# Optimization experiments

Measured on AMD Instinct MI355X. Metric: run time of the kernel, lower is better.

The kernel has to match this reference:

```python
import jax, jax.numpy as jnp
import numpy as np

E = 16        # n_routed_experts
TOP_K = 2
C = 768       # n_embd
I = 1536      # intermediate_size
B, T = 8, 2048


def setup_inputs() -> dict:
    key = jax.random.key(0)
    ks = jax.random.split(key, 9)
    s = 0.02  # init scale
    return {
        "x": jax.random.normal(ks[0], (B, T, C), jnp.float32),
        "w_gate": jax.random.normal(ks[1], (C, E), jnp.float32) * s,
        "expert_bias": jnp.zeros((E,), jnp.float32),
        "wg": jax.random.normal(ks[2], (E, C, I), jnp.float32) * s,
        "wu": jax.random.normal(ks[3], (E, C, I), jnp.float32) * s,
        "wd": jax.random.normal(ks[4], (E, I, C), jnp.float32) * s,
        "swg": jax.random.normal(ks[5], (C, I), jnp.float32) * s,
        "swu": jax.random.normal(ks[6], (C, I), jnp.float32) * s,
        "swd": jax.random.normal(ks[7], (I, C), jnp.float32) * s,
    }


def _expert(x, wg_e, wu_e, wd_e):
    # SwiGLU FFN: down(silu(gate(x)) * up(x))
    return (jax.nn.silu(x @ wg_e) * (x @ wu_e)) @ wd_e


def reference(x, w_gate, expert_bias, wg, wu, wd, swg, swu, swd):
    Bq, Tq, Cq = x.shape
    xf = x.reshape(-1, Cq)  # (N, C)
    n_tok = xf.shape[0]

    # shared experts (1 expert, divided by count=1)
    shared = _expert(xf, swg, swu, swd)

    # router: softmax over (logits + bias), top-k, renormalize
    logits = xf @ w_gate + expert_bias  # (N, E)
    probs = jax.nn.softmax(logits, axis=-1)
    topk_p, topk_i = jax.lax.top_k(probs, TOP_K)
    topk_p = topk_p / jnp.sum(topk_p, axis=-1, keepdims=True)

    # combine weights per expert: zero where expert not selected
    comb = jnp.zeros((n_tok, E), xf.dtype).at[
        jnp.arange(n_tok)[:, None], topk_i
    ].add(topk_p)  # (N, E)

    routed = jnp.zeros_like(xf)
    for e in range(E):  # fixed small expert count
        routed = routed + comb[:, e:e + 1] * _expert(xf, wg[e], wu[e], wd[e])

    return (shared + routed).reshape(Bq, Tq, Cq)
```

## Files before the change

kernel.cpp:

```cpp
#include <hip/hip_runtime.h>

typedef unsigned short u16;
typedef unsigned int u32;
typedef __attribute__((ext_vector_type(4))) float f32x4;
typedef __attribute__((ext_vector_type(8))) short short8;
typedef __attribute__((ext_vector_type(4))) u16 u16x4;
typedef __attribute__((ext_vector_type(8))) u16 u16x8;

#define N_TOK 16384
#define C_DIM 768
#define I_DIM 1536
#define N_EXP 16
#define TM 128
#define BK 64
#define MAXT 400
#define PASS_T 200

#define CI_COUNTS 0
#define CI_STARTS 32
#define CI_NTILES 64
#define CI_TILE_E 128
#define CI_ESLOT 2048
#define CI_TOKW 36864
#define CI_PERM 102400
#define CI_RW 153600

#define XB_OFF  1048576u
#define WGU_OFF 26214400u
#define WDP_OFF 106430464u
#define ACT_OFF 146538496u

__device__ __forceinline__ u16 f2bf(float f) {
  u32 x = __float_as_uint(f);
  return (u16)((x + 0x7FFFu + ((x >> 16) & 1u)) >> 16);
}
__device__ __forceinline__ float bf2f(u16 h) {
  return __uint_as_float(((u32)h) << 16);
}
__device__ __forceinline__ void dma16(const void* g, void* l) {
  __builtin_amdgcn_global_load_lds(
      (const __attribute__((address_space(1))) unsigned int*)g,
      (__attribute__((address_space(3))) unsigned int*)l, 16, 0, 0);
}

__global__ void convert_kernel(const float* __restrict__ wg, const float* __restrict__ wu,
                               const float* __restrict__ wd, const float* __restrict__ swg,
                               const float* __restrict__ swu, const float* __restrict__ swd,
                               u16* __restrict__ wgu, u16* __restrict__ wdp) {
  int bid = blockIdx.x;
  const float* src; u16* dst; int K, N, base_n;
  if (bid < 34 * 48) {
    int m = bid / 48, nb = bid % 48;
    int e = m >> 1, gu = m & 1;
    src = (e < N_EXP) ? ((gu ? wu : wg) + (size_t)e * C_DIM * I_DIM) : (gu ? swu : swg);
    dst = wgu + (size_t)m * (C_DIM * I_DIM);
    K = C_DIM; N = I_DIM; base_n = nb * 32;
  } else {
    int b2 = bid - 34 * 48;
    int e = b2 / 24, nb = b2 % 24;
    src = (e < N_EXP) ? (wd + (size_t)e * I_DIM * C_DIM) : swd;
    dst = wdp + (size_t)e * (I_DIM * C_DIM);
    K = I_DIM; N = C_DIM; base_n = nb * 32;
  }
  int tid = threadIdx.x, lane = tid & 63, wv = tid >> 6;
  int lsub = lane >> 3, lchk = lane & 7;
  int ng = base_n + wv * 8 + lsub;
  int c = lchk ^ (ng & 7);
  const float* s0 = src + ng;
  u16* drow = dst + (size_t)ng * K;
  for (int k0 = 0; k0 < K; k0 += 64) {
    u16x8 o;
#pragma unroll
    for (int j = 0; j < 8; j++)
      o[j] = f2bf(s0[(size_t)(k0 + c * 8 + j) * N]);
    *(u16x8*)&drow[k0 + lchk * 8] = o;
  }
}

__global__ void router_kernel(const float* __restrict__ x, const float* __restrict__ wgate,
                              const float* __restrict__ ebias, int* __restrict__ ctrl,
                              u16* __restrict__ xb) {
  __shared__ float xs[16 * 772];
  __shared__ float wgsT[16 * 772];
  __shared__ float lg[16 * 16];
  int tid = threadIdx.x;
  int tok0 = blockIdx.x * 16;
  const float4* xsrc = (const float4*)(x + (size_t)tok0 * C_DIM);
  const float4* wsrc = (const float4*)wgate;
#pragma unroll
  for (int j = 0; j < 12; j++) {
    int q = tid + j * 256;
    float4 v = xsrc[q];
    int tk = q / 192;
    int c4 = q - tk * 192;
    *(float4*)&xs[tk * 772 + c4 * 4] = v;
    u16x4 o; o.x = f2bf(v.x); o.y = f2bf(v.y); o.z = f2bf(v.z); o.w = f2bf(v.w);
    *(u16x4*)(xb + (size_t)tok0 * C_DIM + (size_t)q * 4) = o;
    float4 w = wsrc[q];
    int c = q >> 2, e0 = (q & 3) * 4;
    wgsT[(e0 + 0) * 772 + c] = w.x;
    wgsT[(e0 + 1) * 772 + c] = w.y;
    wgsT[(e0 + 2) * 772 + c] = w.z;
    wgsT[(e0 + 3) * 772 + c] = w.w;
  }
  __syncthreads();
  int tk = tid >> 4, e = tid & 15;
  float acc = ebias[e];
  const float4* xr = (const float4*)&xs[tk * 772];
  const float4* wr = (const float4*)&wgsT[e * 772];
#pragma unroll 4
  for (int c4 = 0; c4 < 192; c4++) {
    float4 xv = xr[c4], wv = wr[c4];
    acc = fmaf(xv.x, wv.x, fmaf(xv.y, wv.y, fmaf(xv.z, wv.z, fmaf(xv.w, wv.w, acc))));
  }
  lg[tk * 16 + e] = acc;
  __syncthreads();
  if (tid < 16) {
    int n = tok0 + tid;
    float l0 = -1e30f, l1 = -1e30f; int i0 = 0, i1 = 0;
#pragma unroll
    for (int j = 0; j < 16; j++) {
      float l = lg[tid * 16 + j];
      if (l > l0) { l1 = l0; i1 = i0; l0 = l; i0 = j; }
      else if (l > l1) { l1 = l; i1 = j; }
    }
    float e1 = __expf(l1 - l0);
    float inv = 1.f / (1.f + e1);
    int s0 = atomicAdd(&ctrl[CI_COUNTS + i0], 1);
    int s1 = atomicAdd(&ctrl[CI_COUNTS + i1], 1);
    ctrl[CI_ESLOT + 2 * n]     = (i0 << 24) | s0;
    ctrl[CI_ESLOT + 2 * n + 1] = (i1 << 24) | s1;
    float* tw = (float*)(ctrl + CI_TOKW);
    tw[2 * n] = inv; tw[2 * n + 1] = e1 * inv;
  }
}

__global__ void tiles_kernel(int* __restrict__ ctrl) {
  if (threadIdx.x != 0) return;
  int cnt[17];
#pragma unroll
  for (int e = 0; e < 16; e++) cnt[e] = ctrl[CI_COUNTS + e];
  cnt[16] = N_TOK;
  ctrl[CI_COUNTS + 16] = N_TOK;
  int cur = 0, T = 0;
  for (int e = 0; e <= 16; e++) {
    ctrl[CI_STARTS + e] = cur;
    int nt = (cnt[e] + TM - 1) >> 7;
    for (int i = 0; i < nt; i++) ctrl[CI_TILE_E + T++] = e;
    cur += nt << 7;
  }
  ctrl[CI_NTILES] = T;
}

__global__ void scatter_kernel(int* __restrict__ ctrl) {
  int n = blockIdx.x * 256 + threadIdx.x;
  const float* tw = (const float*)(ctrl + CI_TOKW);
  float* rw = (float*)(ctrl + CI_RW);
#pragma unroll
  for (int k = 0; k < 2; k++) {
    int es = ctrl[CI_ESLOT + 2 * n + k];
    int e = es >> 24;
    int slot = es & 0xFFFFFF;
    int row = ctrl[CI_STARTS + e] + slot;
    ctrl[CI_PERM + row] = n;
    rw[row] = tw[2 * n + k];
  }
  int srow = ctrl[CI_STARTS + 16] + n;
  ctrl[CI_PERM + srow] = n;
  rw[srow] = 1.0f;
}

__global__ __launch_bounds__(256, 2)
void gemm1_kernel(const u16* __restrict__ xb, const u16* __restrict__ wgu,
                  u16* __restrict__ act, const int* __restrict__ ctrl, int tile0) {
  __shared__ u16 Al[TM * BK];
  __shared__ u16 Bg[TM * BK];
  __shared__ u16 Bu[TM * BK];
  int t = tile0 + blockIdx.x;
  if (t >= ctrl[CI_NTILES]) return;
  int e = ctrl[CI_TILE_E + t];
  int row0 = t << 7;
  int row0l = blockIdx.x << 7;
  int col0 = blockIdx.y * TM;
  int seg_start = ctrl[CI_STARTS + e];
  bool sh = (e == N_EXP);
  const u16* G = wgu + (size_t)(2 * e) * (C_DIM * I_DIM);
  const u16* U = G + C_DIM * I_DIM;
  int row_lim = sh ? 0x7fffffff : (seg_start + ctrl[CI_COUNTS + e]);
  const int* perm = ctrl + CI_PERM;
  int tid = threadIdx.x;
  int lane = tid & 63, wv = tid >> 6;
  int lsub = lane >> 3;
  int lchk = lane & 7;
  int co = (lchk ^ lsub) * 8;
  const u16* aptr[4];
#pragma unroll
  for (int j = 0; j < 4; j++) {
    int r = row0 + wv * 32 + j * 8 + lsub;
    int tok = sh ? (r - seg_start) : ((r < row_lim) ? perm[r] : 0);
    aptr[j] = xb + (size_t)tok * C_DIM + co;
  }
  size_t boff = (size_t)(col0 + wv * 32 + lsub) * C_DIM + lchk * 8;
  int ldst = wv * 2048;

  f32x4 accg[4][4], accu[4][4];
#pragma unroll
  for (int m = 0; m < 4; m++)
#pragma unroll
    for (int n = 0; n < 4; n++) {
      f32x4 z = {0.f, 0.f, 0.f, 0.f};
      accg[m][n] = z; accu[m][n] = z;
    }
  int lr = lane & 15, lq = lane >> 4;
  int rh = (wv & 1) * 64, chh = (wv >> 1) * 64;

  for (int kk = 0; kk < C_DIM; kk += BK) {
#pragma unroll
    for (int j = 0; j < 4; j++) {
      dma16(aptr[j] + kk,                    Al + ldst + j * 512);
      dma16(G + boff + j * (8 * C_DIM) + kk, Bg + ldst + j * 512);
      dma16(U + boff + j * (8 * C_DIM) + kk, Bu + ldst + j * 512);
    }
    __syncthreads();
#pragma unroll
    for (int s = 0; s < 2; s++) {
      int cidx = s * 4 + lq;
      short8 af[4], bg_[4], bu_[4];
#pragma unroll
      for (int m = 0; m < 4; m++) {
        int r = rh + m * 16 + lr;
        af[m] = *(const short8*)&Al[r * 64 + ((cidx ^ (r & 7)) * 8)];
      }
#pragma unroll
      for (int n = 0; n < 4; n++) {
        int i = chh + n * 16 + lr;
        int off = i * 64 + ((cidx ^ (i & 7)) * 8);
        bg_[n] = *(const short8*)&Bg[off];
        bu_[n] = *(const short8*)&Bu[off];
      }
#pragma unroll
      for (int m = 0; m < 4; m++)
#pragma unroll
        for (int n = 0; n < 4; n++) {
          accg[m][n] = __builtin_amdgcn_mfma_f32_16x16x32_bf16(af[m], bg_[n], accg[m][n], 0, 0, 0);
          accu[m][n] = __builtin_amdgcn_mfma_f32_16x16x32_bf16(af[m], bu_[n], accu[m][n], 0, 0, 0);
        }
    }
    __syncthreads();
  }
#pragma unroll
  for (int m = 0; m < 4; m++)
#pragma unroll
    for (int n = 0; n < 4; n++)
#pragma unroll
      for (int rg = 0; rg < 4; rg++) {
        float g = accg[m][n][rg];
        float h = accu[m][n][rg];
        float a = g * (1.f / (1.f + __expf(-g))) * h;
        int r_loc = rh + m * 16 + lq * 4 + rg;
        int cl = col0 + chh + n * 16 + lr;
        act[(size_t)(row0l + r_loc) * I_DIM + cl] = f2bf(a);
      }
}

__global__ __launch_bounds__(256, 3)
void gemm2_kernel(const u16* __restrict__ act, const u16* __restrict__ wdp,
                  float* __restrict__ out, const int* __restrict__ ctrl, int tile0) {
  __shared__ u16 Al[TM * BK];
  __shared__ u16 Bl[TM * BK];
  int t = tile0 + blockIdx.x;
  if (t >= ctrl[CI_NTILES]) return;
  int e = ctrl[CI_TILE_E + t];
  int row0 = t << 7;
  int row0l = blockIdx.x << 7;
  int col0 = blockIdx.y * TM;
  const u16* D = wdp + (size_t)e * (I_DIM * C_DIM);
  int tid = threadIdx.x;
  int lane = tid & 63, wv = tid >> 6;
  int lsub = lane >> 3, lchk = lane & 7;
  int co = (lchk ^ lsub) * 8;
  const u16* abase = act + (size_t)(row0l + wv * 32 + lsub) * I_DIM + co;
  size_t boff = (size_t)(col0 + wv * 32 + lsub) * I_DIM + lchk * 8;
  int ldst = wv * 2048;

  f32x4 acc[4][4];
#pragma unroll
  for (int m = 0; m < 4; m++)
#pragma unroll
    for (int n = 0; n < 4; n++) {
      f32x4 z = {0.f, 0.f, 0.f, 0.f};
      acc[m][n] = z;
    }
  int lr = lane & 15, lq = lane >> 4;
  int rh = (wv & 1) * 64, chh = (wv >> 1) * 64;

  for (int kk = 0; kk < I_DIM; kk += BK) {
#pragma unroll
    for (int j = 0; j < 4; j++) {
      dma16(abase + (size_t)j * 8 * I_DIM + kk, Al + ldst + j * 512);
      dma16(D + boff + j * (8 * I_DIM) + kk,    Bl + ldst + j * 512);
    }
    __syncthreads();
#pragma unroll
    for (int s = 0; s < 2; s++) {
      int cidx = s * 4 + lq;
      short8 af[4], bf_[4];
#pragma unroll
      for (int m = 0; m < 4; m++) {
        int r = rh + m * 16 + lr;
        af[m] = *(const short8*)&Al[r * 64 + ((cidx ^ (r & 7)) * 8)];
      }
#pragma unroll
      for (int n = 0; n < 4; n++) {
        int i = chh + n * 16 + lr;
        bf_[n] = *(const short8*)&Bl[i * 64 + ((cidx ^ (i & 7)) * 8)];
      }
#pragma unroll
      for (int m = 0; m < 4; m++)
#pragma unroll
        for (int n = 0; n < 4; n++)
          acc[m][n] = __builtin_amdgcn_mfma_f32_16x16x32_bf16(af[m], bf_[n], acc[m][n], 0, 0, 0);
    }
    __syncthreads();
  }
  const int* perm = ctrl + CI_PERM;
  const float* rw = (const float*)(ctrl + CI_RW);
#pragma unroll
  for (int m = 0; m < 4; m++)
#pragma unroll
    for (int rg = 0; rg < 4; rg++) {
      int rgrow = row0 + rh + m * 16 + lq * 4 + rg;
      int tokn = perm[rgrow];
      if (tokn < 0) continue;
      float w = rw[rgrow];
      float* obase = out + (size_t)tokn * C_DIM + col0 + chh + lr;
#pragma unroll
      for (int n = 0; n < 4; n++)
        atomicAdd(obase + n * 16, acc[m][n][rg] * w);
    }
}

extern "C" void kernel_launch(void* const* d_in, const int* in_sizes, int n_in,
                              void* d_out, int out_size, void* d_ws, size_t ws_size,
                              hipStream_t stream) {
  (void)in_sizes; (void)n_in; (void)out_size; (void)ws_size;
  const float* x     = (const float*)d_in[0];
  const float* wgate = (const float*)d_in[1];
  const float* ebias = (const float*)d_in[2];
  const float* wg    = (const float*)d_in[3];
  const float* wu    = (const float*)d_in[4];
  const float* wd    = (const float*)d_in[5];
  const float* swg   = (const float*)d_in[6];
  const float* swu   = (const float*)d_in[7];
  const float* swd   = (const float*)d_in[8];
  float* out = (float*)d_out;
  char* ws = (char*)d_ws;
  int* ctrl = (int*)ws;
  u16* xb  = (u16*)(ws + XB_OFF);
  u16* wgu = (u16*)(ws + WGU_OFF);
  u16* wdp = (u16*)(ws + WDP_OFF);
  u16* act = (u16*)(ws + ACT_OFF);

  hipMemsetAsync(ws, 0, 256, stream);
  hipMemsetAsync(ws + (size_t)CI_PERM * 4, 0xFF, 51200 * 4, stream);
  hipMemsetAsync(d_out, 0, (size_t)N_TOK * C_DIM * 4, stream);
  router_kernel<<<N_TOK / 16, 256, 0, stream>>>(x, wgate, ebias, ctrl, xb);
  tiles_kernel<<<1, 64, 0, stream>>>(ctrl);
  scatter_kernel<<<N_TOK / 256, 256, 0, stream>>>(ctrl);
  convert_kernel<<<34 * 48 + 17 * 24, 256, 0, stream>>>(wg, wu, wd, swg, swu, swd, wgu, wdp);
  for (int p = 0; p < 2; p++) {
    gemm1_kernel<<<dim3(PASS_T, I_DIM / TM), 256, 0, stream>>>(xb, wgu, act, ctrl, p * PASS_T);
    gemm2_kernel<<<dim3(PASS_T, C_DIM / TM), 256, 0, stream>>>(act, wdp, out, ctrl, p * PASS_T);
  }
}
```

Baseline: 1.001 ms.

## Enlarge GEMM tiles to 256 rows, interleave gate/up weights, double-buffer LDS

```diff
diff --git a/kernel.cpp b/kernel.cpp
--- a/kernel.cpp
+++ b/kernel.cpp
@@ -11,10 +11,10 @@
 #define C_DIM 768
 #define I_DIM 1536
 #define N_EXP 16
-#define TM 128
+#define TM 256
 #define BK 64
-#define MAXT 400
-#define PASS_T 200
+#define MAXT 208
+#define PASS_T 104
 
 #define CI_COUNTS 0
 #define CI_STARTS 32
@@ -23,12 +23,15 @@
 #define CI_ESLOT 2048
 #define CI_TOKW 36864
 #define CI_PERM 102400
-#define CI_RW 153600
+#define CI_RW 155648
 
 #define XB_OFF  1048576u
 #define WGU_OFF 26214400u
 #define WDP_OFF 106430464u
 #define ACT_OFF 146538496u
+
+#define BAR() asm volatile("s_barrier" ::: "memory")
+#define WAITVM(N) asm volatile("s_waitcnt vmcnt(" #N ")" ::: "memory")
 
 __device__ __forceinline__ u16 f2bf(float f) {
   u32 x = __float_as_uint(f);
@@ -48,32 +51,39 @@
                                const float* __restrict__ swu, const float* __restrict__ swd,
                                u16* __restrict__ wgu, u16* __restrict__ wdp) {
   int bid = blockIdx.x;
-  const float* src; u16* dst; int K, N, base_n;
-  if (bid < 34 * 48) {
-    int m = bid / 48, nb = bid % 48;
-    int e = m >> 1, gu = m & 1;
-    src = (e < N_EXP) ? ((gu ? wu : wg) + (size_t)e * C_DIM * I_DIM) : (gu ? swu : swg);
-    dst = wgu + (size_t)m * (C_DIM * I_DIM);
-    K = C_DIM; N = I_DIM; base_n = nb * 32;
-  } else {
-    int b2 = bid - 34 * 48;
-    int e = b2 / 24, nb = b2 % 24;
-    src = (e < N_EXP) ? (wd + (size_t)e * I_DIM * C_DIM) : swd;
-    dst = wdp + (size_t)e * (I_DIM * C_DIM);
-    K = I_DIM; N = C_DIM; base_n = nb * 32;
-  }
   int tid = threadIdx.x, lane = tid & 63, wv = tid >> 6;
   int lsub = lane >> 3, lchk = lane & 7;
-  int ng = base_n + wv * 8 + lsub;
-  int c = lchk ^ (ng & 7);
-  const float* s0 = src + ng;
-  u16* drow = dst + (size_t)ng * K;
-  for (int k0 = 0; k0 < K; k0 += 64) {
-    u16x8 o;
-#pragma unroll
-    for (int j = 0; j < 8; j++)
-      o[j] = f2bf(s0[(size_t)(k0 + c * 8 + j) * N]);
-    *(u16x8*)&drow[k0 + lchk * 8] = o;
+  if (bid < 17 * 96) {
+    int e = bid / 96, nb = bid % 96;
+    int ng = nb * 32 + wv * 8 + lsub;
+    int gu = (ng >> 4) & 1;
+    int scol = ((ng >> 5) << 4) | (ng & 15);
+    const float* src = (e < N_EXP) ? ((gu ? wu : wg) + (size_t)e * C_DIM * I_DIM)
+                                   : (gu ? swu : swg);
+    u16* drow = wgu + ((size_t)e * (2 * I_DIM) + ng) * C_DIM;
+    int c = lchk ^ (ng & 7);
+    const float* s0 = src + scol;
+    for (int k0 = 0; k0 < C_DIM; k0 += 64) {
+      u16x8 o;
+#pragma unroll
+      for (int j = 0; j < 8; j++) o[j] = f2bf(s0[(size_t)(k0 + c * 8 + j) * I_DIM]);
+      *(u16x8*)&drow[k0 + lchk * 8] = o;
+    }
+  } else {
+    int b2 = bid - 17 * 96;
+    int e = b2 / 24, nb = b2 % 24;
+    const float* src = (e < N_EXP) ? (wd + (size_t)e * I_DIM * C_DIM) : swd;
+    u16* dst = wdp + (size_t)e * (I_DIM * C_DIM);
+    int ng = nb * 32 + wv * 8 + lsub;
+    int c = lchk ^ (ng & 7);
+    const float* s0 = src + ng;
+    u16* drow = dst + (size_t)ng * I_DIM;
+    for (int k0 = 0; k0 < I_DIM; k0 += 64) {
+      u16x8 o;
+#pragma unroll
+      for (int j = 0; j < 8; j++) o[j] = f2bf(s0[(size_t)(k0 + c * 8 + j) * C_DIM]);
+      *(u16x8*)&drow[k0 + lchk * 8] = o;
+    }
   }
 }
 
@@ -145,9 +155,9 @@
   int cur = 0, T = 0;
   for (int e = 0; e <= 16; e++) {
     ctrl[CI_STARTS + e] = cur;
-    int nt = (cnt[e] + TM - 1) >> 7;
+    int nt = (cnt[e] + TM - 1) >> 8;
     for (int i = 0; i < nt; i++) ctrl[CI_TILE_E + T++] = e;
-    cur += nt << 7;
+    cur += nt << 8;
   }
   ctrl[CI_NTILES] = T;
 }
@@ -170,118 +180,126 @@
   rw[srow] = 1.0f;
 }
 
-__global__ __launch_bounds__(256, 2)
+__global__ __launch_bounds__(512, 2)
 void gemm1_kernel(const u16* __restrict__ xb, const u16* __restrict__ wgu,
                   u16* __restrict__ act, const int* __restrict__ ctrl, int tile0) {
-  __shared__ u16 Al[TM * BK];
-  __shared__ u16 Bg[TM * BK];
-  __shared__ u16 Bu[TM * BK];
-  int t = tile0 + blockIdx.x;
-  if (t >= ctrl[CI_NTILES]) return;
-  int e = ctrl[CI_TILE_E + t];
-  int row0 = t << 7;
-  int row0l = blockIdx.x << 7;
-  int col0 = blockIdx.y * TM;
-  int seg_start = ctrl[CI_STARTS + e];
+  __shared__ u16 As[2][256 * 64];
+  __shared__ u16 Bs[2][256 * 64];
+  int tt = tile0 + blockIdx.x;
+  if (tt >= ctrl[CI_NTILES]) return;
+  int e = ctrl[CI_TILE_E + tt];
+  int row0 = tt << 8;
+  int row0l = blockIdx.x << 8;
+  int col0c = blockIdx.y << 8;
+  int seg = ctrl[CI_STARTS + e];
   bool sh = (e == N_EXP);
-  const u16* G = wgu + (size_t)(2 * e) * (C_DIM * I_DIM);
-  const u16* U = G + C_DIM * I_DIM;
-  int row_lim = sh ? 0x7fffffff : (seg_start + ctrl[CI_COUNTS + e]);
+  const u16* W = wgu + (size_t)e * (2 * I_DIM * C_DIM);
+  int rlim = sh ? 0x7fffffff : (seg + ctrl[CI_COUNTS + e]);
   const int* perm = ctrl + CI_PERM;
   int tid = threadIdx.x;
   int lane = tid & 63, wv = tid >> 6;
-  int lsub = lane >> 3;
-  int lchk = lane & 7;
+  int lsub = lane >> 3, lchk = lane & 7;
   int co = (lchk ^ lsub) * 8;
   const u16* aptr[4];
 #pragma unroll
   for (int j = 0; j < 4; j++) {
     int r = row0 + wv * 32 + j * 8 + lsub;
-    int tok = sh ? (r - seg_start) : ((r < row_lim) ? perm[r] : 0);
+    int tok = sh ? (r - seg) : ((r < rlim) ? perm[r] : 0);
     aptr[j] = xb + (size_t)tok * C_DIM + co;
   }
-  size_t boff = (size_t)(col0 + wv * 32 + lsub) * C_DIM + lchk * 8;
-  int ldst = wv * 2048;
-
-  f32x4 accg[4][4], accu[4][4];
-#pragma unroll
-  for (int m = 0; m < 4; m++)
+  const u16* bptr = W + (size_t)(col0c + wv * 32 + lsub) * C_DIM + lchk * 8;
+  int ldst = (wv * 32 + lsub) * 64 + lchk * 8;
+
+  f32x4 acc[8][4];
+#pragma unroll
+  for (int m = 0; m < 8; m++)
 #pragma unroll
     for (int n = 0; n < 4; n++) {
       f32x4 z = {0.f, 0.f, 0.f, 0.f};
-      accg[m][n] = z; accu[m][n] = z;
+      acc[m][n] = z;
     }
   int lr = lane & 15, lq = lane >> 4;
-  int rh = (wv & 1) * 64, chh = (wv >> 1) * 64;
-
-  for (int kk = 0; kk < C_DIM; kk += BK) {
-#pragma unroll
-    for (int j = 0; j < 4; j++) {
-      dma16(aptr[j] + kk,                    Al + ldst + j * 512);
-      dma16(G + boff + j * (8 * C_DIM) + kk, Bg + ldst + j * 512);
-      dma16(U + boff + j * (8 * C_DIM) + kk, Bu + ldst + j * 512);
-    }
-    __syncthreads();
-#pragma unroll
-    for (int s = 0; s < 2; s++) {
-      int cidx = s * 4 + lq;
-      short8 af[4], bg_[4], bu_[4];
-#pragma unroll
-      for (int m = 0; m < 4; m++) {
-        int r = rh + m * 16 + lr;
-        af[m] = *(const short8*)&Al[r * 64 + ((cidx ^ (r & 7)) * 8)];
+  int wr = wv >> 2, wc = wv & 3;
+
+  auto stage = [&](int kt, int slot) {
+    int kk = kt * BK;
+#pragma unroll
+    for (int j = 0; j < 4; j++) dma16(aptr[j] + kk, &As[slot][ldst + j * 512]);
+#pragma unroll
+    for (int j = 0; j < 4; j++)
+      dma16(bptr + (size_t)j * (8 * C_DIM) + kk, &Bs[slot][ldst + j * 512]);
+  };
+
+  stage(0, 0);
+  stage(1, 1);
+  WAITVM(8);
+  BAR();
+  for (int kt = 0; kt < C_DIM / BK; ++kt) {
+    const u16* Ab = As[kt & 1];
+    const u16* Bb = Bs[kt & 1];
+    __builtin_amdgcn_s_setprio(1);
+#pragma unroll
+    for (int s = 0; s < 2; ++s) {
+      int csh = ((s * 4 + lq) ^ (lr & 7)) * 8;
+      short8 bfr[4];
+#pragma unroll
+      for (int n = 0; n < 4; n++)
+        bfr[n] = *(const short8*)&Bb[(wc * 64 + n * 16 + lr) * 64 + csh];
+#pragma unroll
+      for (int mh = 0; mh < 2; ++mh) {
+        short8 afr[4];
+#pragma unroll
+        for (int mm = 0; mm < 4; mm++)
+          afr[mm] = *(const short8*)&Ab[(wr * 128 + mh * 64 + mm * 16 + lr) * 64 + csh];
+#pragma unroll
+        for (int mm = 0; mm < 4; mm++)
+#pragma unroll
+          for (int n = 0; n < 4; n++)
+            acc[mh * 4 + mm][n] = __builtin_amdgcn_mfma_f32_16x16x32_bf16(
+                afr[mm], bfr[n], acc[mh * 4 + mm][n], 0, 0, 0);
       }
-#pragma unroll
-      for (int n = 0; n < 4; n++) {
-        int i = chh + n * 16 + lr;
-        int off = i * 64 + ((cidx ^ (i & 7)) * 8);
-        bg_[n] = *(const short8*)&Bg[off];
-        bu_[n] = *(const short8*)&Bu[off];
+    }
+    __builtin_amdgcn_s_setprio(0);
+    BAR();
+    if (kt + 2 < C_DIM / BK) { stage(kt + 2, kt & 1); WAITVM(8); }
+    else { WAITVM(0); }
+    BAR();
+  }
+  int cb = (blockIdx.y << 7) + wc * 32;
+#pragma unroll
+  for (int m = 0; m < 8; m++)
+#pragma unroll
+    for (int np = 0; np < 2; np++)
+#pragma unroll
+      for (int rg = 0; rg < 4; rg++) {
+        float g = acc[m][2 * np][rg];
+        float h = acc[m][2 * np + 1][rg];
+        float a = g * (1.f / (1.f + __expf(-g))) * h;
+        int r_loc = wr * 128 + m * 16 + lq * 4 + rg;
+        act[(size_t)(row0l + r_loc) * I_DIM + cb + np * 16 + lr] = f2bf(a);
       }
-#pragma unroll
-      for (int m = 0; m < 4; m++)
-#pragma unroll
-        for (int n = 0; n < 4; n++) {
-          accg[m][n] = __builtin_amdgcn_mfma_f32_16x16x32_bf16(af[m], bg_[n], accg[m][n], 0, 0, 0);
-          accu[m][n] = __builtin_amdgcn_mfma_f32_16x16x32_bf16(af[m], bu_[n], accu[m][n], 0, 0, 0);
-        }
-    }
-    __syncthreads();
-  }
-#pragma unroll
-  for (int m = 0; m < 4; m++)
-#pragma unroll
-    for (int n = 0; n < 4; n++)
-#pragma unroll
-      for (int rg = 0; rg < 4; rg++) {
-        float g = accg[m][n][rg];
-        float h = accu[m][n][rg];
-        float a = g * (1.f / (1.f + __expf(-g))) * h;
-        int r_loc = rh + m * 16 + lq * 4 + rg;
-        int cl = col0 + chh + n * 16 + lr;
-        act[(size_t)(row0l + r_loc) * I_DIM + cl] = f2bf(a);
-      }
-}
-
-__global__ __launch_bounds__(256, 3)
+}
+
+__global__ __launch_bounds__(512, 2)
 void gemm2_kernel(const u16* __restrict__ act, const u16* __restrict__ wdp,
                   float* __restrict__ out, const int* __restrict__ ctrl, int tile0) {
-  __shared__ u16 Al[TM * BK];
-  __shared__ u16 Bl[TM * BK];
-  int t = tile0 + blockIdx.x;
-  if (t >= ctrl[CI_NTILES]) return;
-  int e = ctrl[CI_TILE_E + t];
-  int row0 = t << 7;
-  int row0l = blockIdx.x << 7;
-  int col0 = blockIdx.y * TM;
+  __shared__ u16 As[2][256 * 64];
+  __shared__ u16 Bs[2][128 * 64];
+  int tt = tile0 + blockIdx.x;
+  if (tt >= ctrl[CI_NTILES]) return;
+  int e = ctrl[CI_TILE_E + tt];
+  int row0 = tt << 8;
+  int row0l = blockIdx.x << 8;
+  int col0 = blockIdx.y << 7;
   const u16* D = wdp + (size_t)e * (I_DIM * C_DIM);
   int tid = threadIdx.x;
   int lane = tid & 63, wv = tid >> 6;
   int lsub = lane >> 3, lchk = lane & 7;
   int co = (lchk ^ lsub) * 8;
   const u16* abase = act + (size_t)(row0l + wv * 32 + lsub) * I_DIM + co;
-  size_t boff = (size_t)(col0 + wv * 32 + lsub) * I_DIM + lchk * 8;
-  int ldst = wv * 2048;
+  const u16* bbase = D + (size_t)(col0 + wv * 16 + lsub) * I_DIM + lchk * 8;
+  int ldstA = (wv * 32 + lsub) * 64 + lchk * 8;
+  int ldstB = (wv * 16 + lsub) * 64 + lchk * 8;
 
   f32x4 acc[4][4];
 #pragma unroll
@@ -292,36 +310,47 @@
       acc[m][n] = z;
     }
   int lr = lane & 15, lq = lane >> 4;
-  int rh = (wv & 1) * 64, chh = (wv >> 1) * 64;
-
-  for (int kk = 0; kk < I_DIM; kk += BK) {
-#pragma unroll
-    for (int j = 0; j < 4; j++) {
-      dma16(abase + (size_t)j * 8 * I_DIM + kk, Al + ldst + j * 512);
-      dma16(D + boff + j * (8 * I_DIM) + kk,    Bl + ldst + j * 512);
-    }
-    __syncthreads();
-#pragma unroll
-    for (int s = 0; s < 2; s++) {
-      int cidx = s * 4 + lq;
-      short8 af[4], bf_[4];
-#pragma unroll
-      for (int m = 0; m < 4; m++) {
-        int r = rh + m * 16 + lr;
-        af[m] = *(const short8*)&Al[r * 64 + ((cidx ^ (r & 7)) * 8)];
-      }
-#pragma unroll
-      for (int n = 0; n < 4; n++) {
-        int i = chh + n * 16 + lr;
-        bf_[n] = *(const short8*)&Bl[i * 64 + ((cidx ^ (i & 7)) * 8)];
-      }
+  int wr = wv >> 1, wc = wv & 1;
+
+  auto stage = [&](int kt, int slot) {
+    int kk = kt * BK;
+#pragma unroll
+    for (int j = 0; j < 4; j++)
+      dma16(abase + (size_t)j * (8 * I_DIM) + kk, &As[slot][ldstA + j * 512]);
+#pragma unroll
+    for (int j = 0; j < 2; j++)
+      dma16(bbase + (size_t)j * (8 * I_DIM) + kk, &Bs[slot][ldstB + j * 512]);
+  };
+
+  stage(0, 0);
+  stage(1, 1);
+  WAITVM(6);
+  BAR();
+  for (int kt = 0; kt < I_DIM / BK; ++kt) {
+    const u16* Ab = As[kt & 1];
+    const u16* Bb = Bs[kt & 1];
+    __builtin_amdgcn_s_setprio(1);
+#pragma unroll
+    for (int s = 0; s < 2; ++s) {
+      int csh = ((s * 4 + lq) ^ (lr & 7)) * 8;
+      short8 bfr[4], afr[4];
+#pragma unroll
+      for (int n = 0; n < 4; n++)
+        bfr[n] = *(const short8*)&Bb[(wc * 64 + n * 16 + lr) * 64 + csh];
 #pragma unroll
       for (int m = 0; m < 4; m++)
+        afr[m] = *(const short8*)&Ab[(wr * 64 + m * 16 + lr) * 64 + csh];
+#pragma unroll
+      for (int m = 0; m < 4; m++)
 #pragma unroll
         for (int n = 0; n < 4; n++)
-          acc[m][n] = __builtin_amdgcn_mfma_f32_16x16x32_bf16(af[m], bf_[n], acc[m][n], 0, 0, 0);
-    }
-    __syncthreads();
+          acc[m][n] = __builtin_amdgcn_mfma_f32_16x16x32_bf16(afr[m], bfr[n], acc[m][n], 0, 0, 0);
+    }
+    __builtin_amdgcn_s_setprio(0);
+    BAR();
+    if (kt + 2 < I_DIM / BK) { stage(kt + 2, kt & 1); WAITVM(6); }
+    else { WAITVM(0); }
+    BAR();
   }
   const int* perm = ctrl + CI_PERM;
   const float* rw = (const float*)(ctrl + CI_RW);
@@ -329,11 +358,11 @@
   for (int m = 0; m < 4; m++)
 #pragma unroll
     for (int rg = 0; rg < 4; rg++) {
-      int rgrow = row0 + rh + m * 16 + lq * 4 + rg;
+      int rgrow = row0 + wr * 64 + m * 16 + lq * 4 + rg;
       int tokn = perm[rgrow];
       if (tokn < 0) continue;
       float w = rw[rgrow];
-      float* obase = out + (size_t)tokn * C_DIM + col0 + chh + lr;
+      float* obase = out + (size_t)tokn * C_DIM + col0 + wc * 64 + lr;
 #pragma unroll
       for (int n = 0; n < 4; n++)
         atomicAdd(obase + n * 16, acc[m][n][rg] * w);
@@ -362,14 +391,14 @@
   u16* act = (u16*)(ws + ACT_OFF);
 
   hipMemsetAsync(ws, 0, 256, stream);
-  hipMemsetAsync(ws + (size_t)CI_PERM * 4, 0xFF, 51200 * 4, stream);
+  hipMemsetAsync(ws + (size_t)CI_PERM * 4, 0xFF, 53248 * 4, stream);
   hipMemsetAsync(d_out, 0, (size_t)N_TOK * C_DIM * 4, stream);
   router_kernel<<<N_TOK / 16, 256, 0, stream>>>(x, wgate, ebias, ctrl, xb);
   tiles_kernel<<<1, 64, 0, stream>>>(ctrl);
   scatter_kernel<<<N_TOK / 256, 256, 0, stream>>>(ctrl);
-  convert_kernel<<<34 * 48 + 17 * 24, 256, 0, stream>>>(wg, wu, wd, swg, swu, swd, wgu, wdp);
+  convert_kernel<<<17 * 96 + 17 * 24, 256, 0, stream>>>(wg, wu, wd, swg, swu, swd, wgu, wdp);
   for (int p = 0; p < 2; p++) {
-    gemm1_kernel<<<dim3(PASS_T, I_DIM / TM), 256, 0, stream>>>(xb, wgu, act, ctrl, p * PASS_T);
-    gemm2_kernel<<<dim3(PASS_T, C_DIM / TM), 256, 0, stream>>>(act, wdp, out, ctrl, p * PASS_T);
-  }
-}
+    gemm1_kernel<<<dim3(PASS_T, 2 * I_DIM / 256), 512, 0, stream>>>(xb, wgu, act, ctrl, p * PASS_T);
+    gemm2_kernel<<<dim3(PASS_T, C_DIM / 128), 512, 0, stream>>>(act, wdp, out, ctrl, p * PASS_T);
+  }
+}
```

Result: slower. 1.130 ms (+12.9%).

## Interleave gate/up weight columns so gemm1 runs as one fused wide GEMM

Applied to the files above, without the earlier changes.

```diff
diff --git a/kernel.cpp b/kernel.cpp
--- a/kernel.cpp
+++ b/kernel.cpp
@@ -48,32 +48,39 @@
                                const float* __restrict__ swu, const float* __restrict__ swd,
                                u16* __restrict__ wgu, u16* __restrict__ wdp) {
   int bid = blockIdx.x;
-  const float* src; u16* dst; int K, N, base_n;
-  if (bid < 34 * 48) {
-    int m = bid / 48, nb = bid % 48;
-    int e = m >> 1, gu = m & 1;
-    src = (e < N_EXP) ? ((gu ? wu : wg) + (size_t)e * C_DIM * I_DIM) : (gu ? swu : swg);
-    dst = wgu + (size_t)m * (C_DIM * I_DIM);
-    K = C_DIM; N = I_DIM; base_n = nb * 32;
-  } else {
-    int b2 = bid - 34 * 48;
-    int e = b2 / 24, nb = b2 % 24;
-    src = (e < N_EXP) ? (wd + (size_t)e * I_DIM * C_DIM) : swd;
-    dst = wdp + (size_t)e * (I_DIM * C_DIM);
-    K = I_DIM; N = C_DIM; base_n = nb * 32;
-  }
   int tid = threadIdx.x, lane = tid & 63, wv = tid >> 6;
   int lsub = lane >> 3, lchk = lane & 7;
-  int ng = base_n + wv * 8 + lsub;
-  int c = lchk ^ (ng & 7);
-  const float* s0 = src + ng;
-  u16* drow = dst + (size_t)ng * K;
-  for (int k0 = 0; k0 < K; k0 += 64) {
-    u16x8 o;
-#pragma unroll
-    for (int j = 0; j < 8; j++)
-      o[j] = f2bf(s0[(size_t)(k0 + c * 8 + j) * N]);
-    *(u16x8*)&drow[k0 + lchk * 8] = o;
+  if (bid < 17 * 96) {
+    int e = bid / 96, nb = bid % 96;
+    int ng = nb * 32 + wv * 8 + lsub;
+    int gu = (ng >> 4) & 1;
+    int scol = ((ng >> 5) << 4) | (ng & 15);
+    const float* src = (e < N_EXP) ? ((gu ? wu : wg) + (size_t)e * C_DIM * I_DIM)
+                                   : (gu ? swu : swg);
+    u16* drow = wgu + ((size_t)e * (2 * I_DIM) + ng) * C_DIM;
+    int c = lchk ^ (ng & 7);
+    const float* s0 = src + scol;
+    for (int k0 = 0; k0 < C_DIM; k0 += 64) {
+      u16x8 o;
+#pragma unroll
+      for (int j = 0; j < 8; j++) o[j] = f2bf(s0[(size_t)(k0 + c * 8 + j) * I_DIM]);
+      *(u16x8*)&drow[k0 + lchk * 8] = o;
+    }
+  } else {
+    int b2 = bid - 17 * 96;
+    int e = b2 / 24, nb = b2 % 24;
+    const float* src = (e < N_EXP) ? (wd + (size_t)e * I_DIM * C_DIM) : swd;
+    u16* dst = wdp + (size_t)e * (I_DIM * C_DIM);
+    int ng = nb * 32 + wv * 8 + lsub;
+    int c = lchk ^ (ng & 7);
+    const float* s0 = src + ng;
+    u16* drow = dst + (size_t)ng * I_DIM;
+    for (int k0 = 0; k0 < I_DIM; k0 += 64) {
+      u16x8 o;
+#pragma unroll
+      for (int j = 0; j < 8; j++) o[j] = f2bf(s0[(size_t)(k0 + c * 8 + j) * C_DIM]);
+      *(u16x8*)&drow[k0 + lchk * 8] = o;
+    }
   }
 }
 
@@ -170,22 +177,20 @@
   rw[srow] = 1.0f;
 }
 
-__global__ __launch_bounds__(256, 2)
+__global__ __launch_bounds__(256, 3)
 void gemm1_kernel(const u16* __restrict__ xb, const u16* __restrict__ wgu,
                   u16* __restrict__ act, const int* __restrict__ ctrl, int tile0) {
   __shared__ u16 Al[TM * BK];
-  __shared__ u16 Bg[TM * BK];
-  __shared__ u16 Bu[TM * BK];
+  __shared__ u16 Bl[TM * BK];
   int t = tile0 + blockIdx.x;
   if (t >= ctrl[CI_NTILES]) return;
   int e = ctrl[CI_TILE_E + t];
   int row0 = t << 7;
   int row0l = blockIdx.x << 7;
-  int col0 = blockIdx.y * TM;
+  int col0c = blockIdx.y << 7;
   int seg_start = ctrl[CI_STARTS + e];
   bool sh = (e == N_EXP);
-  const u16* G = wgu + (size_t)(2 * e) * (C_DIM * I_DIM);
-  const u16* U = G + C_DIM * I_DIM;
+  const u16* W = wgu + (size_t)e * (2 * I_DIM) * C_DIM;
   int row_lim = sh ? 0x7fffffff : (seg_start + ctrl[CI_COUNTS + e]);
   const int* perm = ctrl + CI_PERM;
   int tid = threadIdx.x;
@@ -200,16 +205,16 @@
     int tok = sh ? (r - seg_start) : ((r < row_lim) ? perm[r] : 0);
     aptr[j] = xb + (size_t)tok * C_DIM + co;
   }
-  size_t boff = (size_t)(col0 + wv * 32 + lsub) * C_DIM + lchk * 8;
+  size_t boff = (size_t)(col0c + wv * 32 + lsub) * C_DIM + lchk * 8;
   int ldst = wv * 2048;
 
-  f32x4 accg[4][4], accu[4][4];
+  f32x4 acc[4][4];
 #pragma unroll
   for (int m = 0; m < 4; m++)
 #pragma unroll
     for (int n = 0; n < 4; n++) {
       f32x4 z = {0.f, 0.f, 0.f, 0.f};
-      accg[m][n] = z; accu[m][n] = z;
+      acc[m][n] = z;
     }
   int lr = lane & 15, lq = lane >> 4;
   int rh = (wv & 1) * 64, chh = (wv >> 1) * 64;
@@ -218,14 +223,13 @@
 #pragma unroll
     for (int j = 0; j < 4; j++) {
       dma16(aptr[j] + kk,                    Al + ldst + j * 512);
-      dma16(G + boff + j * (8 * C_DIM) + kk, Bg + ldst + j * 512);
-      dma16(U + boff + j * (8 * C_DIM) + kk, Bu + ldst + j * 512);
+      dma16(W + boff + j * (8 * C_DIM) + kk, Bl + ldst + j * 512);
     }
     __syncthreads();
 #pragma unroll
     for (int s = 0; s < 2; s++) {
       int cidx = s * 4 + lq;
-      short8 af[4], bg_[4], bu_[4];
+      short8 af[4], bf_[4];
 #pragma unroll
       for (int m = 0; m < 4; m++) {
         int r = rh + m * 16 + lr;
@@ -234,32 +238,28 @@
 #pragma unroll
       for (int n = 0; n < 4; n++) {
         int i = chh + n * 16 + lr;
-        int off = i * 64 + ((cidx ^ (i & 7)) * 8);
-        bg_[n] = *(const short8*)&Bg[off];
-        bu_[n] = *(const short8*)&Bu[off];
+        bf_[n] = *(const short8*)&Bl[i * 64 + ((cidx ^ (i & 7)) * 8)];
       }
 #pragma unroll
       for (int m = 0; m < 4; m++)
 #pragma unroll
-        for (int n = 0; n < 4; n++) {
-          accg[m][n] = __builtin_amdgcn_mfma_f32_16x16x32_bf16(af[m], bg_[n], accg[m][n], 0, 0, 0);
-          accu[m][n] = __builtin_amdgcn_mfma_f32_16x16x32_bf16(af[m], bu_[n], accu[m][n], 0, 0, 0);
-        }
+        for (int n = 0; n < 4; n++)
+          acc[m][n] = __builtin_amdgcn_mfma_f32_16x16x32_bf16(af[m], bf_[n], acc[m][n], 0, 0, 0);
     }
     __syncthreads();
   }
+  int cbase = (blockIdx.y << 6) + (chh >> 1);
 #pragma unroll
   for (int m = 0; m < 4; m++)
 #pragma unroll
-    for (int n = 0; n < 4; n++)
+    for (int np = 0; np < 2; np++)
 #pragma unroll
       for (int rg = 0; rg < 4; rg++) {
-        float g = accg[m][n][rg];
-        float h = accu[m][n][rg];
+        float g = acc[m][2 * np][rg];
+        float h = acc[m][2 * np + 1][rg];
         float a = g * (1.f / (1.f + __expf(-g))) * h;
         int r_loc = rh + m * 16 + lq * 4 + rg;
-        int cl = col0 + chh + n * 16 + lr;
-        act[(size_t)(row0l + r_loc) * I_DIM + cl] = f2bf(a);
+        act[(size_t)(row0l + r_loc) * I_DIM + cbase + np * 16 + lr] = f2bf(a);
       }
 }
 
@@ -367,9 +367,9 @@
   router_kernel<<<N_TOK / 16, 256, 0, stream>>>(x, wgate, ebias, ctrl, xb);
   tiles_kernel<<<1, 64, 0, stream>>>(ctrl);
   scatter_kernel<<<N_TOK / 256, 256, 0, stream>>>(ctrl);
-  convert_kernel<<<34 * 48 + 17 * 24, 256, 0, stream>>>(wg, wu, wd, swg, swu, swd, wgu, wdp);
+  convert_kernel<<<17 * 96 + 17 * 24, 256, 0, stream>>>(wg, wu, wd, swg, swu, swd, wgu, wdp);
   for (int p = 0; p < 2; p++) {
-    gemm1_kernel<<<dim3(PASS_T, I_DIM / TM), 256, 0, stream>>>(xb, wgu, act, ctrl, p * PASS_T);
+    gemm1_kernel<<<dim3(PASS_T, 2 * I_DIM / TM), 256, 0, stream>>>(xb, wgu, act, ctrl, p * PASS_T);
     gemm2_kernel<<<dim3(PASS_T, C_DIM / TM), 256, 0, stream>>>(act, wdp, out, ctrl, p * PASS_T);
   }
 }
```

Measured after the change: 1.014 ms. Within noise of the previous version (+1.3%).
